# Kernel tuning notes

Hardware: AMD Instinct MI355X
Metric: run time of the kernel (lower is better)

## Reference

```python
import jax, jax.numpy as jnp
import numpy as np

N_NODES = 50000
N_EDGES = 800000
D = 128          # input_node_dim == output_node_dim (residual)
T = 3            # number of node types == number of edge types
NODE_IN = D + T * D  # node updater input dim = 512


def setup_inputs() -> dict:
    key = jax.random.key(0)
    ks = jax.random.split(key, 8)
    scale = 0.05
    return {
        "node_feature": jax.random.normal(ks[0], (N_NODES, D), jnp.float32),
        "W_e": jax.random.normal(ks[1], (T, D, D), jnp.float32) * scale,
        "b_e": jnp.zeros((T, D), jnp.float32),
        "W_n": jax.random.normal(ks[2], (T, D, NODE_IN), jnp.float32) * scale,
        "b_n": jnp.zeros((T, D), jnp.float32),
        "edge_src": jax.random.randint(ks[3], (N_EDGES,), 0, N_NODES, jnp.int32),
        "edge_dst": jax.random.randint(ks[4], (N_EDGES,), 0, N_NODES, jnp.int32),
        "edge_type": jax.random.randint(ks[5], (N_EDGES,), 0, T, jnp.int32),
        "node_type": jax.random.randint(ks[6], (N_NODES,), 0, T, jnp.int32),
    }


def reference(node_feature, W_e, b_e, W_n, b_n, edge_src, edge_dst, edge_type, node_type):
    N, Din = node_feature.shape
    n_types = W_e.shape[0]
    out_dim = W_e.shape[1]

    # message_function: per-edge-type MLP on source features, relu, zero elsewhere
    src = node_feature[edge_src]                      # [E, D] gather
    parts = [jax.nn.relu(node_feature)]               # reduce_function relu's node_feature
    for t in range(n_types):
        msg = jax.nn.relu(src @ W_e[t].T + b_e[t])    # [E, out]
        msg = jnp.where((edge_type == t)[:, None], msg, jnp.zeros((), msg.dtype))
        # mailbox sum over incoming edges per destination node
        parts.append(jax.ops.segment_sum(msg, edge_dst, num_segments=N))
    agg = jnp.concatenate(parts, axis=1)              # [N, D + T*out]

    # per-node-type updater MLP, dispatched by node_type
    updated = jnp.zeros((N, out_dim), node_feature.dtype)
    for t in range(n_types):
        o = agg @ W_n[t].T + b_n[t]                   # [N, out]
        updated = jnp.where((node_type == t)[:, None], o, updated)

    # use_residual = True
    return updated + node_feature
```

## Files before the change

kernel.cpp:

```cpp
#include <hip/hip_runtime.h>
#include <hip/hip_bf16.h>

#define NN 50000
#define NE 800000
#define DD 128
#define NT 3
#define AGGW 384
#define EM 64
#define EM2 128
#define LDK 136
#define CB 32
#define LDK2 520
#define NBITS 7
#define NBINS ((NN + 127) / 128)
#define EPB 2048
#define BINCAP 2560
#define NTILES_MAX (((NN + EM - 1) / EM) + NT)
#define NTILE_PAD (((NTILES_MAX + 7) / 8) * 8)

typedef __bf16 bf16x8 __attribute__((ext_vector_type(8)));
typedef float f32x4 __attribute__((ext_vector_type(4)));
typedef unsigned short u16x8 __attribute__((ext_vector_type(8)));

__device__ __forceinline__ unsigned short f2b(float f) {
    __hip_bfloat16 h = __float2bfloat16(f);
    return __builtin_bit_cast(unsigned short, h);
}
__device__ __forceinline__ float b2f(unsigned int u16bits) {
    unsigned int x = u16bits << 16;
    return __builtin_bit_cast(float, x);
}

__global__ void k_prep(const float* __restrict__ nf, const float* __restrict__ We,
                       const float* __restrict__ Wn, unsigned short* __restrict__ nfb,
                       unsigned short* __restrict__ Web, unsigned short* __restrict__ Wnb,
                       int* __restrict__ bhist, int* __restrict__ cnts) {
    size_t i = (size_t)blockIdx.x * blockDim.x + threadIdx.x;
    if (i < NBINS) bhist[i] = 0;
    if (i >= NBINS && i < NBINS + 16) cnts[i - NBINS] = 0;
    const size_t n0 = (size_t)NN * DD / 8;
    const size_t n1 = (size_t)NT * DD * DD / 8;
    const size_t n2 = (size_t)NT * DD * 512 / 8;
    size_t total = n0 + n1 + n2;
    for (size_t p = i; p < total; p += (size_t)gridDim.x * blockDim.x) {
        const float* s; unsigned short* d; size_t off;
        if (p < n0)            { s = nf; d = nfb; off = p; }
        else if (p < n0 + n1)  { s = We; d = Web; off = p - n0; }
        else                   { s = Wn; d = Wnb; off = p - n0 - n1; }
        const float4* f4 = (const float4*)(s + off * 8);
        float4 x = f4[0], y = f4[1];
        u16x8 u = { f2b(x.x), f2b(x.y), f2b(x.z), f2b(x.w),
                    f2b(y.x), f2b(y.y), f2b(y.z), f2b(y.w) };
        *(u16x8*)(d + off * 8) = u;
    }
}

__global__ __launch_bounds__(256) void k_binhist(const int* __restrict__ edst,
        const int* __restrict__ ntp, int* __restrict__ bhist, int* __restrict__ cnts) {
    __shared__ int lh[NBINS];
    __shared__ int ln[3];
    int tid = threadIdx.x;
    for (int i = tid; i < NBINS; i += 256) lh[i] = 0;
    if (tid < 3) ln[tid] = 0;
    __syncthreads();
    int i0 = blockIdx.x * blockDim.x + tid;
    int stride = gridDim.x * blockDim.x;
    for (int p = i0; p < NE; p += stride) atomicAdd(&lh[edst[p] >> NBITS], 1);
    for (int p = i0; p < NN; p += stride) atomicAdd(&ln[ntp[p]], 1);
    __syncthreads();
    for (int i = tid; i < NBINS; i += 256) if (lh[i]) atomicAdd(&bhist[i], lh[i]);
    if (tid < 3) atomicAdd(&cnts[6 + tid], ln[tid]);
}

__global__ __launch_bounds__(512) void k_binscan(const int* __restrict__ bhist,
        int* __restrict__ binptr, int* __restrict__ bincur, int* __restrict__ rowptr) {
    __shared__ int sa[NBINS], sb[NBINS];
    int tid = threadIdx.x;
    if (tid < NBINS) sa[tid] = bhist[tid];
    __syncthreads();
    int flip = 0;
    for (int off = 1; off < NBINS; off <<= 1) {
        int* src = flip ? sb : sa;
        int* dst = flip ? sa : sb;
        if (tid < NBINS) dst[tid] = src[tid] + ((tid >= off) ? src[tid - off] : 0);
        __syncthreads();
        flip ^= 1;
    }
    int* inc = flip ? sb : sa;
    if (tid < NBINS) {
        int excl = (tid == 0) ? 0 : inc[tid - 1];
        binptr[tid] = excl;
        bincur[tid] = excl;
    }
    if (tid == 0) { binptr[NBINS] = NE; rowptr[NN] = NE; }
}

__global__ __launch_bounds__(256) void k_binscatter(const int* __restrict__ esrc,
        const int* __restrict__ edst, const int* __restrict__ et,
        const int* __restrict__ ntp, int* __restrict__ bincur, int* __restrict__ cnts,
        int* __restrict__ pe, int* __restrict__ sn) {
    const int NEB = (NE + EPB - 1) / EPB;
    __shared__ int lh[NBINS], gb[NBINS], lr[NBINS];
    __shared__ int lcnt[3], lbase[3];
    int tid = threadIdx.x, b = blockIdx.x;
    if (b < NEB) {
        for (int i = tid; i < NBINS; i += 256) { lh[i] = 0; lr[i] = 0; }
        __syncthreads();
        int e0 = b * EPB;
        for (int i = 0; i < EPB; i += 256) {
            int e = e0 + i + tid;
            if (e < NE) atomicAdd(&lh[edst[e] >> NBITS], 1);
        }
        __syncthreads();
        for (int i = tid; i < NBINS; i += 256)
            if (lh[i]) gb[i] = atomicAdd(&bincur[i], lh[i]);
        __syncthreads();
        for (int i = 0; i < EPB; i += 256) {
            int e = e0 + i + tid;
            if (e < NE) {
                int d = edst[e];
                int t = et[e];
                int bin = d >> NBITS;
                int rank = atomicAdd(&lr[bin], 1);
                pe[gb[bin] + rank] = (t * NN + esrc[e]) | ((d & 127) << 18) | (t << 25);
            }
        }
    } else {
        if (tid < 3) lcnt[tid] = 0;
        __syncthreads();
        int p = (b - NEB) * 256 + tid;
        int t = -1, rank = 0;
        if (p < NN) { t = ntp[p]; rank = atomicAdd(&lcnt[t], 1); }
        __syncthreads();
        if (tid < 3) lbase[tid] = atomicAdd(&cnts[9 + tid], lcnt[tid]);
        __syncthreads();
        if (p < NN) {
            int c0 = cnts[6], c1 = cnts[7];
            int off = (t == 0) ? 0 : (t == 1) ? c0 : c0 + c1;
            sn[off + lbase[t] + rank] = p;
        }
    }
}

__global__ __launch_bounds__(256) void k_binsort(const int* __restrict__ binptr,
        int* __restrict__ pe, int* __restrict__ rowptr) {
    __shared__ int lcnt[128], lrk[128], lrp[128];
    __shared__ unsigned int sorted[BINCAP];
    int b = blockIdx.x, tid = threadIdx.x;
    int beg = binptr[b], end = binptr[b + 1];
    int cnt = min(end - beg, BINCAP);
    if (tid < 128) { lcnt[tid] = 0; lrk[tid] = 0; }
    __syncthreads();
    for (int e = tid; e < cnt; e += 256)
        atomicAdd(&lcnt[(pe[beg + e] >> 18) & 127], 1);
    __syncthreads();
    if (tid < 64) {
        int v = lcnt[2 * tid] + lcnt[2 * tid + 1];
        int s = v;
        for (int d = 1; d < 64; d <<= 1) {
            int u = __shfl_up(s, d);
            if (tid >= d) s += u;
        }
        int excl = s - v;
        lrp[2 * tid] = excl;
        lrp[2 * tid + 1] = excl + lcnt[2 * tid];
    }
    __syncthreads();
    if (tid < 128) {
        int node = b * 128 + tid;
        if (node < NN) rowptr[node] = beg + lrp[tid];
    }
    for (int e = tid; e < cnt; e += 256) {
        unsigned int p = pe[beg + e];
        int d = (p >> 18) & 127;
        int pos = lrp[d] + atomicAdd(&lrk[d], 1);
        sorted[pos] = p;
    }
    __syncthreads();
    for (int e = tid; e < cnt; e += 256) pe[beg + e] = sorted[e];
}

__global__ __launch_bounds__(512, 4) void k_msg(const unsigned short* __restrict__ nfb,
        const unsigned short* __restrict__ Web, const float* __restrict__ be,
        unsigned short* __restrict__ M) {
    __shared__ unsigned short Wsm[DD][LDK];
    const int TILES = (NN + EM2 - 1) / EM2;
    int b = blockIdx.x;
    int t = b / TILES, tile = b % TILES;
    int base = tile * EM2;
    int m = min(EM2, NN - base);
    int tid = threadIdx.x;
    {
        int row = tid >> 2, c0 = (tid & 3) * 32;
        const u16x8* src = (const u16x8*)(Web + ((size_t)t * DD + row) * DD + c0);
#pragma unroll
        for (int v = 0; v < 4; ++v) *(u16x8*)&Wsm[row][c0 + v * 8] = src[v];
    }
    __syncthreads();

    int wave = tid >> 6, l = tid & 63, lr = l & 15, kg = l >> 4;
    int arow = min(base + wave * 16 + lr, NN - 1);
    const u16x8* Arow = (const u16x8*)(nfb + (size_t)arow * DD);
    f32x4 acc[8];
#pragma unroll
    for (int n = 0; n < 8; n++) acc[n] = (f32x4){0.f, 0.f, 0.f, 0.f};
#pragma unroll
    for (int k0 = 0; k0 < DD; k0 += 32) {
        bf16x8 a = __builtin_bit_cast(bf16x8, Arow[(k0 >> 3) + kg]);
#pragma unroll
        for (int n = 0; n < 8; n++) {
            bf16x8 bb = *(const bf16x8*)&Wsm[n * 16 + lr][k0 + kg * 8];
            acc[n] = __builtin_amdgcn_mfma_f32_16x16x32_bf16(a, bb, acc[n], 0, 0, 0);
        }
    }
    unsigned short* Mt = M + (size_t)t * NN * DD;
#pragma unroll
    for (int n = 0; n < 8; n++) {
        int col = n * 16 + lr;
        float bias = be[t * DD + col];
#pragma unroll
        for (int r = 0; r < 4; r++) {
            int row = wave * 16 + kg * 4 + r;
            if (row < m) {
                float v = acc[n][r] + bias;
                Mt[(size_t)(base + row) * DD + col] = f2b(fmaxf(v, 0.f));
            }
        }
    }
}

__global__ __launch_bounds__(128) void k_agg(const unsigned short* __restrict__ M,
        const int* __restrict__ rowptr, const int* __restrict__ pe,
        unsigned short* __restrict__ aggb) {
    int node = blockIdx.x * 8 + (threadIdx.x >> 4);
    int q = threadIdx.x & 15;
    int beg = rowptr[node], end = rowptr[node + 1];
    const uint4* Mu4 = (const uint4*)M;
    float a0[8] = {0,0,0,0,0,0,0,0};
    float a1[8] = {0,0,0,0,0,0,0,0};
    float a2[8] = {0,0,0,0,0,0,0,0};
    int e = beg;
    while (e < end) {
        unsigned int p[8];
        uint4 v[8];
#pragma unroll
        for (int j = 0; j < 8; ++j) p[j] = pe[min(e + j, end - 1)];
#pragma unroll
        for (int j = 0; j < 8; ++j)
            if (e + j < end) v[j] = Mu4[(size_t)(p[j] & 0x3FFFFu) * 16 + q];
#pragma unroll
        for (int j = 0; j < 8; ++j) {
            if (e + j < end) {
                int t = p[j] >> 25;
                float f0 = b2f(v[j].x & 0xFFFF), f1 = b2f(v[j].x >> 16);
                float f2 = b2f(v[j].y & 0xFFFF), f3 = b2f(v[j].y >> 16);
                float f4 = b2f(v[j].z & 0xFFFF), f5 = b2f(v[j].z >> 16);
                float f6 = b2f(v[j].w & 0xFFFF), f7 = b2f(v[j].w >> 16);
                if (t == 0) {
                    a0[0] += f0; a0[1] += f1; a0[2] += f2; a0[3] += f3;
                    a0[4] += f4; a0[5] += f5; a0[6] += f6; a0[7] += f7;
                } else if (t == 1) {
                    a1[0] += f0; a1[1] += f1; a1[2] += f2; a1[3] += f3;
                    a1[4] += f4; a1[5] += f5; a1[6] += f6; a1[7] += f7;
                } else {
                    a2[0] += f0; a2[1] += f1; a2[2] += f2; a2[3] += f3;
                    a2[4] += f4; a2[5] += f5; a2[6] += f6; a2[7] += f7;
                }
            }
        }
        e += 8;
    }
    unsigned int* dst = (unsigned int*)(aggb + (size_t)node * AGGW);
    uint4 o0 = { (unsigned int)f2b(a0[0]) | ((unsigned int)f2b(a0[1]) << 16),
                 (unsigned int)f2b(a0[2]) | ((unsigned int)f2b(a0[3]) << 16),
                 (unsigned int)f2b(a0[4]) | ((unsigned int)f2b(a0[5]) << 16),
                 (unsigned int)f2b(a0[6]) | ((unsigned int)f2b(a0[7]) << 16) };
    uint4 o1 = { (unsigned int)f2b(a1[0]) | ((unsigned int)f2b(a1[1]) << 16),
                 (unsigned int)f2b(a1[2]) | ((unsigned int)f2b(a1[3]) << 16),
                 (unsigned int)f2b(a1[4]) | ((unsigned int)f2b(a1[5]) << 16),
                 (unsigned int)f2b(a1[6]) | ((unsigned int)f2b(a1[7]) << 16) };
    uint4 o2 = { (unsigned int)f2b(a2[0]) | ((unsigned int)f2b(a2[1]) << 16),
                 (unsigned int)f2b(a2[2]) | ((unsigned int)f2b(a2[3]) << 16),
                 (unsigned int)f2b(a2[4]) | ((unsigned int)f2b(a2[5]) << 16),
                 (unsigned int)f2b(a2[6]) | ((unsigned int)f2b(a2[7]) << 16) };
    ((uint4*)dst)[q]        = o0;
    ((uint4*)(dst + 64))[q] = o1;
    ((uint4*)(dst + 128))[q] = o2;
}

__global__ __launch_bounds__(256, 3) void k_node(const float* __restrict__ nf,
        const unsigned short* __restrict__ nfb, const unsigned short* __restrict__ Wnb,
        const float* __restrict__ bn, const int* __restrict__ sn,
        const int* __restrict__ cnts, const unsigned short* __restrict__ aggb,
        float* __restrict__ out) {
    __shared__ unsigned short Wsm[CB][LDK2];
    int c0 = cnts[6], c1 = cnts[7], c2 = cnts[8];
    int n0 = (c0 + EM - 1) / EM, n1 = (c1 + EM - 1) / EM, n2 = (c2 + EM - 1) / EM;
    int ntile = n0 + n1 + n2;
    int b = blockIdx.x;
    int rt = (b & 7) * (NTILE_PAD / 8) + (b >> 3);
    if (rt >= ntile) return;
    int tid = threadIdx.x;
    int wave = tid >> 6, l = tid & 63, lr = l & 15, kg = l >> 4;
    int t, tile;
    if (rt < n0) { t = 0; tile = rt; }
    else if (rt < n0 + n1) { t = 1; tile = rt - n0; }
    else { t = 2; tile = rt - n0 - n1; }
    int off = (t == 0) ? 0 : (t == 1) ? c0 : c0 + c1;
    int cntt = (t == 0) ? c0 : (t == 1) ? c1 : c2;
    int base = off + tile * EM;
    int m = min(EM, cntt - tile * EM);

    int myrow = sn[base + min(wave * 16 + lr, m - 1)];
    const u16x8* An = (const u16x8*)(nfb + (size_t)myrow * DD);
    const u16x8* Ag = (const u16x8*)(aggb + (size_t)myrow * AGGW);
    u16x8 afr[16];
#pragma unroll
    for (int kc = 0; kc < 4; ++kc) {
#pragma unroll
        for (int k0 = 0; k0 < DD; k0 += 32) {
            u16x8 araw;
            if (kc == 0) {
                araw = An[(k0 >> 3) + kg];
#pragma unroll
                for (int j = 0; j < 8; ++j)
                    araw[j] = (araw[j] & 0x8000) ? (unsigned short)0 : araw[j];
            } else {
                araw = Ag[((kc - 1) * DD + k0) / 8 + kg];
            }
            afr[kc * 4 + (k0 >> 5)] = araw;
        }
    }

    int nd[4];
#pragma unroll
    for (int r = 0; r < 4; ++r) nd[r] = sn[base + min(wave * 16 + kg * 4 + r, m - 1)];

    int srow = tid & 31, scc = (tid >> 5) * 64;
#pragma unroll 1
    for (int cbk = 0; cbk < 4; ++cbk) {
        if (cbk) __syncthreads();
        const u16x8* src = (const u16x8*)(Wnb + ((size_t)t * DD + cbk * CB + srow) * 512 + scc);
#pragma unroll
        for (int v = 0; v < 8; ++v) *(u16x8*)&Wsm[srow][scc + v * 8] = src[v];
        __syncthreads();

        f32x4 acc0 = {0.f, 0.f, 0.f, 0.f}, acc1 = {0.f, 0.f, 0.f, 0.f};
#pragma unroll
        for (int kc = 0; kc < 4; ++kc) {
#pragma unroll
            for (int k0 = 0; k0 < DD; k0 += 32) {
                bf16x8 a = __builtin_bit_cast(bf16x8, afr[kc * 4 + (k0 >> 5)]);
                int kw = kc * DD + k0 + kg * 8;
                bf16x8 b0 = *(const bf16x8*)&Wsm[lr][kw];
                bf16x8 b1 = *(const bf16x8*)&Wsm[16 + lr][kw];
                acc0 = __builtin_amdgcn_mfma_f32_16x16x32_bf16(a, b0, acc0, 0, 0, 0);
                acc1 = __builtin_amdgcn_mfma_f32_16x16x32_bf16(a, b1, acc1, 0, 0, 0);
            }
        }
#pragma unroll
        for (int n = 0; n < 2; n++) {
            int col = cbk * CB + n * 16 + lr;
            float bias = bn[t * DD + col];
            const f32x4& av = n ? acc1 : acc0;
#pragma unroll
            for (int r = 0; r < 4; r++) {
                int row = wave * 16 + kg * 4 + r;
                if (row < m) {
                    int node = nd[r];
                    out[(size_t)node * DD + col] = av[r] + bias + nf[(size_t)node * DD + col];
                }
            }
        }
    }
}

extern "C" void kernel_launch(void* const* d_in, const int* in_sizes, int n_in,
                              void* d_out, int out_size, void* d_ws, size_t ws_size,
                              hipStream_t stream) {
    const float* nf   = (const float*)d_in[0];
    const float* We   = (const float*)d_in[1];
    const float* be   = (const float*)d_in[2];
    const float* Wn   = (const float*)d_in[3];
    const float* bn   = (const float*)d_in[4];
    const int*   esrc = (const int*)d_in[5];
    const int*   edst = (const int*)d_in[6];
    const int*   et   = (const int*)d_in[7];
    const int*   ntp  = (const int*)d_in[8];
    float* out = (float*)d_out;

    char* w = (char*)d_ws;
    unsigned short* M    = (unsigned short*)w;  w += (size_t)NT * NN * DD * 2;
    unsigned short* aggb = (unsigned short*)w;  w += (size_t)NN * AGGW * 2;
    unsigned short* nfb  = (unsigned short*)w;  w += (size_t)NN * DD * 2;
    unsigned short* Web  = (unsigned short*)w;  w += (size_t)NT * DD * DD * 2;
    unsigned short* Wnb  = (unsigned short*)w;  w += (size_t)NT * DD * 512 * 2;
    int* pe     = (int*)w;  w += (size_t)NE * 4;
    int* bhist  = (int*)w;  w += (NBINS + 1) * 4;
    int* binptr = (int*)w;  w += (NBINS + 1) * 4;
    int* bincur = (int*)w;  w += (NBINS + 1) * 4;
    int* rowptr = (int*)w;  w += (size_t)(NN + 1) * 4;
    int* sn     = (int*)w;  w += (size_t)NN * 4;
    int* cnts   = (int*)w;  w += 16 * 4;

    const int NEB = (NE + EPB - 1) / EPB;
    const int NCH = (NN + 255) / 256;
    const int TILES2 = (NN + EM2 - 1) / EM2;

    k_prep<<<1024, 256, 0, stream>>>(nf, We, Wn, nfb, Web, Wnb, bhist, cnts);
    k_binhist<<<256, 256, 0, stream>>>(edst, ntp, bhist, cnts);
    k_binscan<<<1, 512, 0, stream>>>(bhist, binptr, bincur, rowptr);
    k_binscatter<<<NEB + NCH, 256, 0, stream>>>(esrc, edst, et, ntp, bincur, cnts, pe, sn);
    k_binsort<<<NBINS, 256, 0, stream>>>(binptr, pe, rowptr);
    k_msg<<<NT * TILES2, 512, 0, stream>>>(nfb, Web, be, M);
    k_agg<<<NN / 8, 128, 0, stream>>>(M, rowptr, pe, aggb);
    k_node<<<NTILE_PAD, 256, 0, stream>>>(nf, nfb, Wnb, bn, sn, cnts, aggb, out);
}
```

Before: 148.7 us.

## Fuse edge histogram into prep kernel and add nontemporal loads/stores

```diff
diff --git a/kernel.cpp b/kernel.cpp
--- a/kernel.cpp
+++ b/kernel.cpp
@@ -17,10 +17,14 @@
 #define BINCAP 2560
 #define NTILES_MAX (((NN + EM - 1) / EM) + NT)
 #define NTILE_PAD (((NTILES_MAX + 7) / 8) * 8)
+#define HIST_BLOCKS 128
+#define EPH (NE / HIST_BLOCKS)
+#define NPH ((NN + HIST_BLOCKS - 1) / HIST_BLOCKS)
 
 typedef __bf16 bf16x8 __attribute__((ext_vector_type(8)));
 typedef float f32x4 __attribute__((ext_vector_type(4)));
 typedef unsigned short u16x8 __attribute__((ext_vector_type(8)));
+typedef unsigned int u32x4 __attribute__((ext_vector_type(4)));
 
 __device__ __forceinline__ unsigned short f2b(float f) {
     __hip_bfloat16 h = __float2bfloat16(f);
@@ -31,18 +35,29 @@
     return __builtin_bit_cast(float, x);
 }
 
-__global__ void k_prep(const float* __restrict__ nf, const float* __restrict__ We,
-                       const float* __restrict__ Wn, unsigned short* __restrict__ nfb,
-                       unsigned short* __restrict__ Web, unsigned short* __restrict__ Wnb,
-                       int* __restrict__ bhist, int* __restrict__ cnts) {
-    size_t i = (size_t)blockIdx.x * blockDim.x + threadIdx.x;
-    if (i < NBINS) bhist[i] = 0;
-    if (i >= NBINS && i < NBINS + 16) cnts[i - NBINS] = 0;
+__global__ __launch_bounds__(256) void k_prep(const float* __restrict__ nf,
+        const float* __restrict__ We, const float* __restrict__ Wn,
+        unsigned short* __restrict__ nfb, unsigned short* __restrict__ Web,
+        unsigned short* __restrict__ Wnb, const int* __restrict__ edst,
+        const int* __restrict__ ntp, int* __restrict__ bpart, int* __restrict__ npart) {
+    __shared__ int lh[NBINS];
+    __shared__ int ln[3];
+    int tid = threadIdx.x, b = blockIdx.x;
+    bool hist = (b < HIST_BLOCKS);
+    if (hist) {
+        for (int i = tid; i < NBINS; i += 256) lh[i] = 0;
+        if (tid < 3) ln[tid] = 0;
+        __syncthreads();
+        int e0 = b * EPH;
+        for (int i = tid; i < EPH; i += 256) atomicAdd(&lh[edst[e0 + i] >> NBITS], 1);
+        int p0 = b * NPH, p1 = min(NN, p0 + NPH);
+        for (int p = p0 + tid; p < p1; p += 256) atomicAdd(&ln[ntp[p]], 1);
+    }
     const size_t n0 = (size_t)NN * DD / 8;
     const size_t n1 = (size_t)NT * DD * DD / 8;
     const size_t n2 = (size_t)NT * DD * 512 / 8;
     size_t total = n0 + n1 + n2;
-    for (size_t p = i; p < total; p += (size_t)gridDim.x * blockDim.x) {
+    for (size_t p = (size_t)b * 256 + tid; p < total; p += (size_t)gridDim.x * 256) {
         const float* s; unsigned short* d; size_t off;
         if (p < n0)            { s = nf; d = nfb; off = p; }
         else if (p < n0 + n1)  { s = We; d = Web; off = p - n0; }
@@ -53,36 +68,34 @@
                     f2b(y.x), f2b(y.y), f2b(y.z), f2b(y.w) };
         *(u16x8*)(d + off * 8) = u;
     }
-}
-
-__global__ __launch_bounds__(256) void k_binhist(const int* __restrict__ edst,
-        const int* __restrict__ ntp, int* __restrict__ bhist, int* __restrict__ cnts) {
-    __shared__ int lh[NBINS];
-    __shared__ int ln[3];
+    if (hist) {
+        __syncthreads();
+        for (int i = tid; i < NBINS; i += 256) bpart[b * NBINS + i] = lh[i];
+        if (tid < 3) npart[b * 3 + tid] = ln[tid];
+    }
+}
+
+__global__ __launch_bounds__(512) void k_binscan(const int* __restrict__ bpart,
+        const int* __restrict__ npart, int* __restrict__ binptr, int* __restrict__ bincur,
+        int* __restrict__ rowptr, int* __restrict__ cnts) {
+    __shared__ int sa[512], sb[512];
     int tid = threadIdx.x;
-    for (int i = tid; i < NBINS; i += 256) lh[i] = 0;
-    if (tid < 3) ln[tid] = 0;
-    __syncthreads();
-    int i0 = blockIdx.x * blockDim.x + tid;
-    int stride = gridDim.x * blockDim.x;
-    for (int p = i0; p < NE; p += stride) atomicAdd(&lh[edst[p] >> NBITS], 1);
-    for (int p = i0; p < NN; p += stride) atomicAdd(&ln[ntp[p]], 1);
-    __syncthreads();
-    for (int i = tid; i < NBINS; i += 256) if (lh[i]) atomicAdd(&bhist[i], lh[i]);
-    if (tid < 3) atomicAdd(&cnts[6 + tid], ln[tid]);
-}
-
-__global__ __launch_bounds__(512) void k_binscan(const int* __restrict__ bhist,
-        int* __restrict__ binptr, int* __restrict__ bincur, int* __restrict__ rowptr) {
-    __shared__ int sa[NBINS], sb[NBINS];
-    int tid = threadIdx.x;
-    if (tid < NBINS) sa[tid] = bhist[tid];
+    int v = 0;
+    if (tid < NBINS)
+        for (int h = 0; h < HIST_BLOCKS; ++h) v += bpart[h * NBINS + tid];
+    sa[tid] = v;
+    if (tid < 3) {
+        int s = 0;
+        for (int h = 0; h < HIST_BLOCKS; ++h) s += npart[h * 3 + tid];
+        cnts[6 + tid] = s;
+        cnts[9 + tid] = 0;
+    }
     __syncthreads();
     int flip = 0;
-    for (int off = 1; off < NBINS; off <<= 1) {
+    for (int off = 1; off < 512; off <<= 1) {
         int* src = flip ? sb : sa;
         int* dst = flip ? sa : sb;
-        if (tid < NBINS) dst[tid] = src[tid] + ((tid >= off) ? src[tid - off] : 0);
+        dst[tid] = src[tid] + ((tid >= off) ? src[tid - off] : 0);
         __syncthreads();
         flip ^= 1;
     }
@@ -235,16 +248,16 @@
     int node = blockIdx.x * 8 + (threadIdx.x >> 4);
     int q = threadIdx.x & 15;
     int beg = rowptr[node], end = rowptr[node + 1];
-    const uint4* Mu4 = (const uint4*)M;
+    const u32x4* Mu4 = (const u32x4*)M;
     float a0[8] = {0,0,0,0,0,0,0,0};
     float a1[8] = {0,0,0,0,0,0,0,0};
     float a2[8] = {0,0,0,0,0,0,0,0};
     int e = beg;
     while (e < end) {
         unsigned int p[8];
-        uint4 v[8];
-#pragma unroll
-        for (int j = 0; j < 8; ++j) p[j] = pe[min(e + j, end - 1)];
+        u32x4 v[8];
+#pragma unroll
+        for (int j = 0; j < 8; ++j) p[j] = __builtin_nontemporal_load(&pe[min(e + j, end - 1)]);
 #pragma unroll
         for (int j = 0; j < 8; ++j)
             if (e + j < end) v[j] = Mu4[(size_t)(p[j] & 0x3FFFFu) * 16 + q];
@@ -252,10 +265,10 @@
         for (int j = 0; j < 8; ++j) {
             if (e + j < end) {
                 int t = p[j] >> 25;
-                float f0 = b2f(v[j].x & 0xFFFF), f1 = b2f(v[j].x >> 16);
-                float f2 = b2f(v[j].y & 0xFFFF), f3 = b2f(v[j].y >> 16);
-                float f4 = b2f(v[j].z & 0xFFFF), f5 = b2f(v[j].z >> 16);
-                float f6 = b2f(v[j].w & 0xFFFF), f7 = b2f(v[j].w >> 16);
+                float f0 = b2f(v[j][0] & 0xFFFF), f1 = b2f(v[j][0] >> 16);
+                float f2 = b2f(v[j][1] & 0xFFFF), f3 = b2f(v[j][1] >> 16);
+                float f4 = b2f(v[j][2] & 0xFFFF), f5 = b2f(v[j][2] >> 16);
+                float f6 = b2f(v[j][3] & 0xFFFF), f7 = b2f(v[j][3] >> 16);
                 if (t == 0) {
                     a0[0] += f0; a0[1] += f1; a0[2] += f2; a0[3] += f3;
                     a0[4] += f4; a0[5] += f5; a0[6] += f6; a0[7] += f7;
@@ -271,21 +284,21 @@
         e += 8;
     }
     unsigned int* dst = (unsigned int*)(aggb + (size_t)node * AGGW);
-    uint4 o0 = { (unsigned int)f2b(a0[0]) | ((unsigned int)f2b(a0[1]) << 16),
+    u32x4 o0 = { (unsigned int)f2b(a0[0]) | ((unsigned int)f2b(a0[1]) << 16),
                  (unsigned int)f2b(a0[2]) | ((unsigned int)f2b(a0[3]) << 16),
                  (unsigned int)f2b(a0[4]) | ((unsigned int)f2b(a0[5]) << 16),
                  (unsigned int)f2b(a0[6]) | ((unsigned int)f2b(a0[7]) << 16) };
-    uint4 o1 = { (unsigned int)f2b(a1[0]) | ((unsigned int)f2b(a1[1]) << 16),
+    u32x4 o1 = { (unsigned int)f2b(a1[0]) | ((unsigned int)f2b(a1[1]) << 16),
                  (unsigned int)f2b(a1[2]) | ((unsigned int)f2b(a1[3]) << 16),
                  (unsigned int)f2b(a1[4]) | ((unsigned int)f2b(a1[5]) << 16),
                  (unsigned int)f2b(a1[6]) | ((unsigned int)f2b(a1[7]) << 16) };
-    uint4 o2 = { (unsigned int)f2b(a2[0]) | ((unsigned int)f2b(a2[1]) << 16),
+    u32x4 o2 = { (unsigned int)f2b(a2[0]) | ((unsigned int)f2b(a2[1]) << 16),
                  (unsigned int)f2b(a2[2]) | ((unsigned int)f2b(a2[3]) << 16),
                  (unsigned int)f2b(a2[4]) | ((unsigned int)f2b(a2[5]) << 16),
                  (unsigned int)f2b(a2[6]) | ((unsigned int)f2b(a2[7]) << 16) };
-    ((uint4*)dst)[q]        = o0;
-    ((uint4*)(dst + 64))[q] = o1;
-    ((uint4*)(dst + 128))[q] = o2;
+    __builtin_nontemporal_store(o0, (u32x4*)dst + q);
+    __builtin_nontemporal_store(o1, (u32x4*)(dst + 64) + q);
+    __builtin_nontemporal_store(o2, (u32x4*)(dst + 128) + q);
 }
 
 __global__ __launch_bounds__(256, 3) void k_node(const float* __restrict__ nf,
@@ -368,7 +381,9 @@
                 int row = wave * 16 + kg * 4 + r;
                 if (row < m) {
                     int node = nd[r];
-                    out[(size_t)node * DD + col] = av[r] + bias + nf[(size_t)node * DD + col];
+                    float nfv = __builtin_nontemporal_load(&nf[(size_t)node * DD + col]);
+                    __builtin_nontemporal_store(av[r] + bias + nfv,
+                                                &out[(size_t)node * DD + col]);
                 }
             }
         }
@@ -396,7 +411,8 @@
     unsigned short* Web  = (unsigned short*)w;  w += (size_t)NT * DD * DD * 2;
     unsigned short* Wnb  = (unsigned short*)w;  w += (size_t)NT * DD * 512 * 2;
     int* pe     = (int*)w;  w += (size_t)NE * 4;
-    int* bhist  = (int*)w;  w += (NBINS + 1) * 4;
+    int* bpart  = (int*)w;  w += (size_t)HIST_BLOCKS * NBINS * 4;
+    int* npart  = (int*)w;  w += (size_t)HIST_BLOCKS * 3 * 4;
     int* binptr = (int*)w;  w += (NBINS + 1) * 4;
     int* bincur = (int*)w;  w += (NBINS + 1) * 4;
     int* rowptr = (int*)w;  w += (size_t)(NN + 1) * 4;
@@ -407,9 +423,8 @@
     const int NCH = (NN + 255) / 256;
     const int TILES2 = (NN + EM2 - 1) / EM2;
 
-    k_prep<<<1024, 256, 0, stream>>>(nf, We, Wn, nfb, Web, Wnb, bhist, cnts);
-    k_binhist<<<256, 256, 0, stream>>>(edst, ntp, bhist, cnts);
-    k_binscan<<<1, 512, 0, stream>>>(bhist, binptr, bincur, rowptr);
+    k_prep<<<1024, 256, 0, stream>>>(nf, We, Wn, nfb, Web, Wnb, edst, ntp, bpart, npart);
+    k_binscan<<<1, 512, 0, stream>>>(bpart, npart, binptr, bincur, rowptr, cnts);
     k_binscatter<<<NEB + NCH, 256, 0, stream>>>(esrc, edst, et, ntp, bincur, cnts, pe, sn);
     k_binsort<<<NBINS, 256, 0, stream>>>(binptr, pe, rowptr);
     k_msg<<<NT * TILES2, 512, 0, stream>>>(nfb, Web, be, M);
```

Measured after the change: 170.7 us. 14.8% more time.

## Merge edge binscatter and message GEMM into one heterogeneous launch

Applied to the files above, without the earlier changes.

```diff
diff --git a/kernel.cpp b/kernel.cpp
--- a/kernel.cpp
+++ b/kernel.cpp
@@ -21,6 +21,7 @@
 typedef __bf16 bf16x8 __attribute__((ext_vector_type(8)));
 typedef float f32x4 __attribute__((ext_vector_type(4)));
 typedef unsigned short u16x8 __attribute__((ext_vector_type(8)));
+typedef unsigned int u32x4 __attribute__((ext_vector_type(4)));
 
 __device__ __forceinline__ unsigned short f2b(float f) {
     __hip_bfloat16 h = __float2bfloat16(f);
@@ -95,27 +96,37 @@
     if (tid == 0) { binptr[NBINS] = NE; rowptr[NN] = NE; }
 }
 
-__global__ __launch_bounds__(256) void k_binscatter(const int* __restrict__ esrc,
-        const int* __restrict__ edst, const int* __restrict__ et,
-        const int* __restrict__ ntp, int* __restrict__ bincur, int* __restrict__ cnts,
+__global__ __launch_bounds__(512) void k_mid(
+        const unsigned short* __restrict__ nfb, const unsigned short* __restrict__ Web,
+        const float* __restrict__ be, unsigned short* __restrict__ M,
+        const int* __restrict__ esrc, const int* __restrict__ edst,
+        const int* __restrict__ et, const int* __restrict__ ntp,
+        int* __restrict__ bincur, int* __restrict__ cnts,
         int* __restrict__ pe, int* __restrict__ sn) {
     const int NEB = (NE + EPB - 1) / EPB;
-    __shared__ int lh[NBINS], gb[NBINS], lr[NBINS];
-    __shared__ int lcnt[3], lbase[3];
+    const int NCH2 = (NN + 511) / 512;
+    const int TILES = (NN + EM2 - 1) / EM2;
+    __shared__ unsigned short Wsm[DD][LDK];
     int tid = threadIdx.x, b = blockIdx.x;
+
     if (b < NEB) {
-        for (int i = tid; i < NBINS; i += 256) { lh[i] = 0; lr[i] = 0; }
+        int* lh = (int*)&Wsm[0][0];
+        int* gb = lh + NBINS;
+        int* lr = gb + NBINS;
+        for (int i = tid; i < NBINS; i += 512) { lh[i] = 0; lr[i] = 0; }
         __syncthreads();
         int e0 = b * EPB;
-        for (int i = 0; i < EPB; i += 256) {
+#pragma unroll
+        for (int i = 0; i < EPB; i += 512) {
             int e = e0 + i + tid;
             if (e < NE) atomicAdd(&lh[edst[e] >> NBITS], 1);
         }
         __syncthreads();
-        for (int i = tid; i < NBINS; i += 256)
+        for (int i = tid; i < NBINS; i += 512)
             if (lh[i]) gb[i] = atomicAdd(&bincur[i], lh[i]);
         __syncthreads();
-        for (int i = 0; i < EPB; i += 256) {
+#pragma unroll
+        for (int i = 0; i < EPB; i += 512) {
             int e = e0 + i + tid;
             if (e < NE) {
                 int d = edst[e];
@@ -125,10 +136,12 @@
                 pe[gb[bin] + rank] = (t * NN + esrc[e]) | ((d & 127) << 18) | (t << 25);
             }
         }
-    } else {
+    } else if (b < NEB + NCH2) {
+        int* lcnt = (int*)&Wsm[0][0];
+        int* lbase = lcnt + 4;
         if (tid < 3) lcnt[tid] = 0;
         __syncthreads();
-        int p = (b - NEB) * 256 + tid;
+        int p = (b - NEB) * 512 + tid;
         int t = -1, rank = 0;
         if (p < NN) { t = ntp[p]; rank = atomicAdd(&lcnt[t], 1); }
         __syncthreads();
@@ -138,6 +151,48 @@
             int c0 = cnts[6], c1 = cnts[7];
             int off = (t == 0) ? 0 : (t == 1) ? c0 : c0 + c1;
             sn[off + lbase[t] + rank] = p;
+        }
+    } else {
+        int bb = b - NEB - NCH2;
+        int t = bb / TILES, tile = bb % TILES;
+        int base = tile * EM2;
+        int m = min(EM2, NN - base);
+        {
+            int row = tid >> 2, c0 = (tid & 3) * 32;
+            const u16x8* src = (const u16x8*)(Web + ((size_t)t * DD + row) * DD + c0);
+#pragma unroll
+            for (int v = 0; v < 4; ++v) *(u16x8*)&Wsm[row][c0 + v * 8] = src[v];
+        }
+        __syncthreads();
+
+        int wave = tid >> 6, l = tid & 63, lr2 = l & 15, kg = l >> 4;
+        int arow = min(base + wave * 16 + lr2, NN - 1);
+        const u16x8* Arow = (const u16x8*)(nfb + (size_t)arow * DD);
+        f32x4 acc[8];
+#pragma unroll
+        for (int n = 0; n < 8; n++) acc[n] = (f32x4){0.f, 0.f, 0.f, 0.f};
+#pragma unroll
+        for (int k0 = 0; k0 < DD; k0 += 32) {
+            bf16x8 a = __builtin_bit_cast(bf16x8, Arow[(k0 >> 3) + kg]);
+#pragma unroll
+            for (int n = 0; n < 8; n++) {
+                bf16x8 bbv = *(const bf16x8*)&Wsm[n * 16 + lr2][k0 + kg * 8];
+                acc[n] = __builtin_amdgcn_mfma_f32_16x16x32_bf16(a, bbv, acc[n], 0, 0, 0);
+            }
+        }
+        unsigned short* Mt = M + (size_t)t * NN * DD;
+#pragma unroll
+        for (int n = 0; n < 8; n++) {
+            int col = n * 16 + lr2;
+            float bias = be[t * DD + col];
+#pragma unroll
+            for (int r = 0; r < 4; r++) {
+                int row = wave * 16 + kg * 4 + r;
+                if (row < m) {
+                    float v = acc[n][r] + bias;
+                    Mt[(size_t)(base + row) * DD + col] = f2b(fmaxf(v, 0.f));
+                }
+            }
         }
     }
 }
@@ -180,69 +235,20 @@
     for (int e = tid; e < cnt; e += 256) pe[beg + e] = sorted[e];
 }
 
-__global__ __launch_bounds__(512, 4) void k_msg(const unsigned short* __restrict__ nfb,
-        const unsigned short* __restrict__ Web, const float* __restrict__ be,
-        unsigned short* __restrict__ M) {
-    __shared__ unsigned short Wsm[DD][LDK];
-    const int TILES = (NN + EM2 - 1) / EM2;
-    int b = blockIdx.x;
-    int t = b / TILES, tile = b % TILES;
-    int base = tile * EM2;
-    int m = min(EM2, NN - base);
-    int tid = threadIdx.x;
-    {
-        int row = tid >> 2, c0 = (tid & 3) * 32;
-        const u16x8* src = (const u16x8*)(Web + ((size_t)t * DD + row) * DD + c0);
-#pragma unroll
-        for (int v = 0; v < 4; ++v) *(u16x8*)&Wsm[row][c0 + v * 8] = src[v];
-    }
-    __syncthreads();
-
-    int wave = tid >> 6, l = tid & 63, lr = l & 15, kg = l >> 4;
-    int arow = min(base + wave * 16 + lr, NN - 1);
-    const u16x8* Arow = (const u16x8*)(nfb + (size_t)arow * DD);
-    f32x4 acc[8];
-#pragma unroll
-    for (int n = 0; n < 8; n++) acc[n] = (f32x4){0.f, 0.f, 0.f, 0.f};
-#pragma unroll
-    for (int k0 = 0; k0 < DD; k0 += 32) {
-        bf16x8 a = __builtin_bit_cast(bf16x8, Arow[(k0 >> 3) + kg]);
-#pragma unroll
-        for (int n = 0; n < 8; n++) {
-            bf16x8 bb = *(const bf16x8*)&Wsm[n * 16 + lr][k0 + kg * 8];
-            acc[n] = __builtin_amdgcn_mfma_f32_16x16x32_bf16(a, bb, acc[n], 0, 0, 0);
-        }
-    }
-    unsigned short* Mt = M + (size_t)t * NN * DD;
-#pragma unroll
-    for (int n = 0; n < 8; n++) {
-        int col = n * 16 + lr;
-        float bias = be[t * DD + col];
-#pragma unroll
-        for (int r = 0; r < 4; r++) {
-            int row = wave * 16 + kg * 4 + r;
-            if (row < m) {
-                float v = acc[n][r] + bias;
-                Mt[(size_t)(base + row) * DD + col] = f2b(fmaxf(v, 0.f));
-            }
-        }
-    }
-}
-
 __global__ __launch_bounds__(128) void k_agg(const unsigned short* __restrict__ M,
         const int* __restrict__ rowptr, const int* __restrict__ pe,
         unsigned short* __restrict__ aggb) {
     int node = blockIdx.x * 8 + (threadIdx.x >> 4);
     int q = threadIdx.x & 15;
     int beg = rowptr[node], end = rowptr[node + 1];
-    const uint4* Mu4 = (const uint4*)M;
+    const u32x4* Mu4 = (const u32x4*)M;
     float a0[8] = {0,0,0,0,0,0,0,0};
     float a1[8] = {0,0,0,0,0,0,0,0};
     float a2[8] = {0,0,0,0,0,0,0,0};
     int e = beg;
     while (e < end) {
         unsigned int p[8];
-        uint4 v[8];
+        u32x4 v[8];
 #pragma unroll
         for (int j = 0; j < 8; ++j) p[j] = pe[min(e + j, end - 1)];
 #pragma unroll
@@ -252,10 +258,10 @@
         for (int j = 0; j < 8; ++j) {
             if (e + j < end) {
                 int t = p[j] >> 25;
-                float f0 = b2f(v[j].x & 0xFFFF), f1 = b2f(v[j].x >> 16);
-                float f2 = b2f(v[j].y & 0xFFFF), f3 = b2f(v[j].y >> 16);
-                float f4 = b2f(v[j].z & 0xFFFF), f5 = b2f(v[j].z >> 16);
-                float f6 = b2f(v[j].w & 0xFFFF), f7 = b2f(v[j].w >> 16);
+                float f0 = b2f(v[j][0] & 0xFFFF), f1 = b2f(v[j][0] >> 16);
+                float f2 = b2f(v[j][1] & 0xFFFF), f3 = b2f(v[j][1] >> 16);
+                float f4 = b2f(v[j][2] & 0xFFFF), f5 = b2f(v[j][2] >> 16);
+                float f6 = b2f(v[j][3] & 0xFFFF), f7 = b2f(v[j][3] >> 16);
                 if (t == 0) {
                     a0[0] += f0; a0[1] += f1; a0[2] += f2; a0[3] += f3;
                     a0[4] += f4; a0[5] += f5; a0[6] += f6; a0[7] += f7;
@@ -271,21 +277,21 @@
         e += 8;
     }
     unsigned int* dst = (unsigned int*)(aggb + (size_t)node * AGGW);
-    uint4 o0 = { (unsigned int)f2b(a0[0]) | ((unsigned int)f2b(a0[1]) << 16),
+    u32x4 o0 = { (unsigned int)f2b(a0[0]) | ((unsigned int)f2b(a0[1]) << 16),
                  (unsigned int)f2b(a0[2]) | ((unsigned int)f2b(a0[3]) << 16),
                  (unsigned int)f2b(a0[4]) | ((unsigned int)f2b(a0[5]) << 16),
                  (unsigned int)f2b(a0[6]) | ((unsigned int)f2b(a0[7]) << 16) };
-    uint4 o1 = { (unsigned int)f2b(a1[0]) | ((unsigned int)f2b(a1[1]) << 16),
+    u32x4 o1 = { (unsigned int)f2b(a1[0]) | ((unsigned int)f2b(a1[1]) << 16),
                  (unsigned int)f2b(a1[2]) | ((unsigned int)f2b(a1[3]) << 16),
                  (unsigned int)f2b(a1[4]) | ((unsigned int)f2b(a1[5]) << 16),
                  (unsigned int)f2b(a1[6]) | ((unsigned int)f2b(a1[7]) << 16) };
-    uint4 o2 = { (unsigned int)f2b(a2[0]) | ((unsigned int)f2b(a2[1]) << 16),
+    u32x4 o2 = { (unsigned int)f2b(a2[0]) | ((unsigned int)f2b(a2[1]) << 16),
                  (unsigned int)f2b(a2[2]) | ((unsigned int)f2b(a2[3]) << 16),
                  (unsigned int)f2b(a2[4]) | ((unsigned int)f2b(a2[5]) << 16),
                  (unsigned int)f2b(a2[6]) | ((unsigned int)f2b(a2[7]) << 16) };
-    ((uint4*)dst)[q]        = o0;
-    ((uint4*)(dst + 64))[q] = o1;
-    ((uint4*)(dst + 128))[q] = o2;
+    ((u32x4*)dst)[q]        = o0;
+    ((u32x4*)(dst + 64))[q] = o1;
+    ((u32x4*)(dst + 128))[q] = o2;
 }
 
 __global__ __launch_bounds__(256, 3) void k_node(const float* __restrict__ nf,
@@ -404,15 +410,15 @@
     int* cnts   = (int*)w;  w += 16 * 4;
 
     const int NEB = (NE + EPB - 1) / EPB;
-    const int NCH = (NN + 255) / 256;
+    const int NCH2 = (NN + 511) / 512;
     const int TILES2 = (NN + EM2 - 1) / EM2;
 
     k_prep<<<1024, 256, 0, stream>>>(nf, We, Wn, nfb, Web, Wnb, bhist, cnts);
     k_binhist<<<256, 256, 0, stream>>>(edst, ntp, bhist, cnts);
     k_binscan<<<1, 512, 0, stream>>>(bhist, binptr, bincur, rowptr);
-    k_binscatter<<<NEB + NCH, 256, 0, stream>>>(esrc, edst, et, ntp, bincur, cnts, pe, sn);
+    k_mid<<<NEB + NCH2 + NT * TILES2, 512, 0, stream>>>(nfb, Web, be, M,
+            esrc, edst, et, ntp, bincur, cnts, pe, sn);
     k_binsort<<<NBINS, 256, 0, stream>>>(binptr, pe, rowptr);
-    k_msg<<<NT * TILES2, 512, 0, stream>>>(nfb, Web, be, M);
     k_agg<<<NN / 8, 128, 0, stream>>>(M, rowptr, pe, aggb);
     k_node<<<NTILE_PAD, 256, 0, stream>>>(nf, nfb, Wnb, bn, sn, cnts, aggb, out);
 }
```

Measured after the change: 138.1 us. 7.1% less time.
